# Performance work log

Hardware: AMD Instinct MI355X
Metric: run time of the kernel (lower is better)

## Reference

```python
import jax, jax.numpy as jnp
import numpy as np

B, D = 32768, 1024


def setup_inputs() -> dict:
    key = jax.random.key(0)
    kx, k1, k2, k3 = jax.random.split(key, 4)
    x = jax.random.normal(kx, (B, D), dtype=jnp.float32)
    w1 = jax.random.normal(k1, (D, D), dtype=jnp.float32) * 0.1
    w2 = jax.random.normal(k2, (D, D), dtype=jnp.float32) * 0.1
    w3 = jax.random.normal(k3, (D, D), dtype=jnp.float32) * 0.1
    return {"x": x, "w1": w1, "w2": w2, "w3": w3}


def reference(x, w1, w2, w3):
    # Order 1: plain dense projection
    r1 = jnp.matmul(x, w1)  # [B, D]

    dim = x.shape[1]
    k = int(dim * 0.1)
    # Select top-k facets by mean |x| over the batch
    _, idx = jax.lax.top_k(jnp.abs(x).mean(axis=0), k)  # [k]
    mask = jnp.zeros((dim,), dtype=x.dtype).at[idx].set(1.0)  # [D]

    x_sparse = x * mask  # [B, D], zero outside active facets
    # Order 2: masked matmul, gated elementwise by the sparse input
    r2 = jnp.matmul(x_sparse, w2) * x_sparse
    # Order 3: masked matmul squared, gated elementwise
    r3 = jnp.square(jnp.matmul(x_sparse, w3)) * x_sparse
    return (r1, r2, r3)
```

## Files before the change

kernel.cpp:

```cpp
#include <hip/hip_runtime.h>
#include <hip/hip_bf16.h>
#include <stdint.h>

#define B_ROWS 32768
#define DIM    1024
#define KACT   102
#define KPAD   104

typedef short bf16x8 __attribute__((ext_vector_type(8)));
typedef float f32x4  __attribute__((ext_vector_type(4)));

__device__ __forceinline__ unsigned short f2bf(float f) {
  union { float f; unsigned u; } v; v.f = f;
  unsigned u = v.u;
  unsigned r = u + 0x7fffu + ((u >> 16) & 1u);
  return (unsigned short)(r >> 16);
}

#define GLDS(g, l) __builtin_amdgcn_global_load_lds( \
    (__attribute__((address_space(1))) void*)(g),    \
    (__attribute__((address_space(3))) void*)(l), 16, 0, 0)

__global__ __launch_bounds__(256) void k_conv(
    const float* __restrict__ x, unsigned short* __restrict__ xb,
    float* __restrict__ partial) {
  const int t  = threadIdx.x;
  const int c0 = t * 4;
  const size_t base = (size_t)blockIdx.x * 64 * DIM;
  float s0 = 0.f, s1 = 0.f, s2 = 0.f, s3 = 0.f;
  #pragma unroll 4
  for (int j = 0; j < 64; ++j) {
    size_t off = base + (size_t)j * DIM + c0;
    float4 v = *(const float4*)(x + off);
    s0 += fabsf(v.x); s1 += fabsf(v.y); s2 += fabsf(v.z); s3 += fabsf(v.w);
    ushort4 o;
    o.x = f2bf(v.x); o.y = f2bf(v.y); o.z = f2bf(v.z); o.w = f2bf(v.w);
    *(ushort4*)(xb + off) = o;
  }
  float4 p; p.x = s0; p.y = s1; p.z = s2; p.w = s3;
  *(float4*)(partial + (size_t)blockIdx.x * DIM + c0) = p;
}

__global__ __launch_bounds__(256) void k_w1t(const float* __restrict__ w1,
                                             unsigned short* __restrict__ w1t) {
  __shared__ unsigned short tile[64][65];
  const int t  = threadIdx.x;
  const int bx = blockIdx.x & 15;
  const int by = blockIdx.x >> 4;
  for (int e = t; e < 64 * 64; e += 256) {
    int r = e >> 6, c = e & 63;
    tile[r][c] = f2bf(w1[(size_t)(by * 64 + r) * DIM + bx * 64 + c]);
  }
  __syncthreads();
  for (int e = t; e < 64 * 64; e += 256) {
    int c = e >> 6, r = e & 63;
    w1t[(size_t)(bx * 64 + c) * DIM + by * 64 + r] = tile[r][c];
  }
}

__global__ __launch_bounds__(128) void k_reduce1(const float* __restrict__ partial,
                                                 float* __restrict__ p2) {
  const int c  = (blockIdx.x & 7) * 128 + threadIdx.x;
  const int ks = blockIdx.x >> 3;
  float s = 0.f;
  #pragma unroll 8
  for (int p = ks * 64; p < ks * 64 + 64; ++p) s += partial[(size_t)p * DIM + c];
  p2[ks * DIM + c] = s;
}

__global__ __launch_bounds__(256) void k_rank(const float* __restrict__ p2,
                                              int* __restrict__ flags) {
  __shared__ double sv[DIM];
  const int t = threadIdx.x;
  for (int e = t; e < DIM; e += 256) {
    double s = 0.0;
    #pragma unroll
    for (int ks = 0; ks < 8; ++ks) s += (double)p2[ks * DIM + e];
    sv[e] = s;
  }
  __syncthreads();
  const int d = blockIdx.x * 256 + t;
  const double sd = sv[d];
  int rank = 0;
  for (int j = 0; j < DIM; ++j) {
    double s = sv[j];
    rank += (s > sd || (s == sd && j < d)) ? 1 : 0;
  }
  flags[d] = (rank < KACT) ? 1 : 0;
}

__global__ __launch_bounds__(1024) void k_compact(const int* __restrict__ flags,
                                                  int* __restrict__ act,
                                                  int* __restrict__ cmap) {
  __shared__ int wcnt[16];
  const int d = threadIdx.x;
  const int f = flags[d];
  unsigned long long m = __ballot(f != 0);
  const int lane = d & 63, w = d >> 6;
  if (lane == 0) wcnt[w] = __popcll(m);
  __syncthreads();
  int off = 0;
  for (int i = 0; i < w; ++i) off += wcnt[i];
  int pos = off + __popcll(m & ((1ull << lane) - 1ull));
  cmap[d] = f ? pos : -1;
  if (f) act[pos] = d;
}

__global__ __launch_bounds__(128) void k_wsub(const float* __restrict__ w2,
                                              const float* __restrict__ w3,
                                              const int* __restrict__ act,
                                              float* __restrict__ W2sub,
                                              float* __restrict__ W3sub) {
  const int i = blockIdx.x;
  const int j = threadIdx.x;
  if (j >= KPAD) return;
  float v2 = 0.f, v3 = 0.f;
  if (i < KACT && j < KACT) {
    size_t o = (size_t)act[i] * DIM + act[j];
    v2 = w2[o]; v3 = w3[o];
  }
  W2sub[i * KPAD + j] = v2;
  W3sub[i * KPAD + j] = v3;
}

#define VMW4 asm volatile("s_waitcnt vmcnt(4)" ::: "memory")
#define VMW0 asm volatile("s_waitcnt vmcnt(0)" ::: "memory")
#define NOP_ (void)0

#define STAGE_A(KT) do { \
  GLDS(Abase + (size_t)sr0 * 1024 + (KT) * 32 + sc0 * 8, &Asl[((KT)&3)*8192 + p0*8]); \
  GLDS(Abase + (size_t)sr1 * 1024 + (KT) * 32 + sc1 * 8, &Asl[((KT)&3)*8192 + p1*8]); \
} while (0)
#define STAGE_B(KT) do { \
  GLDS(Bbase + (size_t)sr0 * 1024 + (KT) * 32 + sc0 * 8, &Bsl[((KT)&3)*8192 + p0*8]); \
  GLDS(Bbase + (size_t)sr1 * 1024 + (KT) * 32 + sc1 * 8, &Bsl[((KT)&3)*8192 + p1*8]); \
} while (0)

#define PH0(SLOT, STAGE_STMT) do { \
  _Pragma("unroll") for (int i = 0; i < 4; ++i) \
    areg[i] = *(const bf16x8*)(&Asl[(SLOT)*8192 + aoff0 + i * 512]); \
  _Pragma("unroll") for (int i = 0; i < 4; ++i) \
    breg[i] = *(const bf16x8*)(&Bsl[(SLOT)*8192 + boff0 + i * 512]); \
  STAGE_STMT; \
  __builtin_amdgcn_s_barrier(); \
  __builtin_amdgcn_s_setprio(1); \
  _Pragma("unroll") for (int mi = 0; mi < 4; ++mi) \
  _Pragma("unroll") for (int ni = 0; ni < 4; ++ni) \
    acc[mi][ni] = __builtin_amdgcn_mfma_f32_16x16x32_bf16(areg[mi], breg[ni], acc[mi][ni], 0, 0, 0); \
  __builtin_amdgcn_s_setprio(0); \
  __builtin_amdgcn_s_barrier(); \
} while (0)

#define PH1(SLOT, STAGE_STMT, WAIT_STMT) do { \
  _Pragma("unroll") for (int i = 0; i < 4; ++i) \
    areg[i] = *(const bf16x8*)(&Asl[(SLOT)*8192 + aoff0 + 2048 + i * 512]); \
  STAGE_STMT; \
  WAIT_STMT; \
  __builtin_amdgcn_s_barrier(); \
  __builtin_amdgcn_s_setprio(1); \
  _Pragma("unroll") for (int mi = 0; mi < 4; ++mi) \
  _Pragma("unroll") for (int ni = 0; ni < 4; ++ni) \
    acc[4 + mi][ni] = __builtin_amdgcn_mfma_f32_16x16x32_bf16(areg[mi], breg[ni], acc[4 + mi][ni], 0, 0, 0); \
  __builtin_amdgcn_s_setprio(0); \
  __builtin_amdgcn_s_barrier(); \
} while (0)

__global__ __launch_bounds__(512, 1) void k_gemm_r1(
    const unsigned short* __restrict__ A,
    const unsigned short* __restrict__ Bt,
    float* __restrict__ C) {
  __shared__ unsigned short Asl[4 * 8192];
  __shared__ unsigned short Bsl[4 * 8192];

  const int t    = threadIdx.x;
  const int lane = t & 63;
  const int wave = t >> 6;
  const int wm   = wave >> 2;
  const int wn   = wave & 3;
  const int la   = lane & 15;
  const int kg   = lane >> 4;
  const int kgx  = kg ^ ((la >> 1) & 3);

  const int swz  = (blockIdx.x & 7) * 64 + (blockIdx.x >> 3);
  const int brow = swz >> 2;
  const int bcol = swz & 3;

  const unsigned short* Abase = A  + (size_t)brow * 256 * 1024;
  const unsigned short* Bbase = Bt + (size_t)bcol * 256 * 1024;

  const int p0 = t, p1 = t + 512;
  const int q0 = p0 ^ ((p0 >> 3) & 3);
  const int q1 = p1 ^ ((p1 >> 3) & 3);
  const int sr0 = q0 >> 2, sc0 = q0 & 3;
  const int sr1 = q1 >> 2, sc1 = q1 & 3;

  const int aoff0 = (wm * 128 + la) * 32 + kgx * 8;
  const int boff0 = (wn * 64  + la) * 32 + kgx * 8;

  f32x4 acc[8][4];
  #pragma unroll
  for (int mi = 0; mi < 8; ++mi)
    #pragma unroll
    for (int ni = 0; ni < 4; ++ni)
      acc[mi][ni] = (f32x4){0.f, 0.f, 0.f, 0.f};

  bf16x8 areg[4], breg[4];

  STAGE_A(0); STAGE_B(0); STAGE_A(1); STAGE_B(1);
  VMW4;
  __builtin_amdgcn_s_barrier();

  for (int kt4 = 0; kt4 < 28; kt4 += 4) {
    PH0(0, STAGE_A(kt4 + 2)); PH1(0, STAGE_B(kt4 + 2), VMW4);
    PH0(1, STAGE_A(kt4 + 3)); PH1(1, STAGE_B(kt4 + 3), VMW4);
    PH0(2, STAGE_A(kt4 + 4)); PH1(2, STAGE_B(kt4 + 4), VMW4);
    PH0(3, STAGE_A(kt4 + 5)); PH1(3, STAGE_B(kt4 + 5), VMW4);
  }
  PH0(0, STAGE_A(30)); PH1(0, STAGE_B(30), VMW4);
  PH0(1, STAGE_A(31)); PH1(1, STAGE_B(31), VMW4);
  PH0(2, NOP_);        PH1(2, NOP_, VMW0);
  PH0(3, NOP_);        PH1(3, NOP_, NOP_);

  const int orow0 = brow * 256 + wm * 128 + (lane >> 4) * 4;
  const int ocol0 = bcol * 256 + wn * 64 + la;
  #pragma unroll
  for (int mi = 0; mi < 8; ++mi)
    #pragma unroll
    for (int ni = 0; ni < 4; ++ni)
      #pragma unroll
      for (int r = 0; r < 4; ++r)
        C[(size_t)(orow0 + mi * 16 + r) * DIM + ocol0 + ni * 16] = acc[mi][ni][r];
}

__global__ __launch_bounds__(512) void k_r23(const float* __restrict__ x,
                                             const float* __restrict__ W2sub,
                                             const float* __restrict__ W3sub,
                                             const int* __restrict__ cmap,
                                             float* __restrict__ out2,
                                             float* __restrict__ out3) {
  __shared__ float W2s[KPAD * KPAD];
  __shared__ float W3s[KPAD * KPAD];
  __shared__ float xs[2][16 * KPAD];
  __shared__ float r2s[16 * KPAD];
  __shared__ float r3s[16 * KPAD];
  __shared__ int   cms[DIM];
  const int t    = threadIdx.x;
  const int row0 = blockIdx.x * 128;

  for (int e = t; e < KPAD * KPAD; e += 512) { W2s[e] = W2sub[e]; W3s[e] = W3sub[e]; }
  for (int e = t; e < DIM; e += 512) cms[e] = cmap[e];
  for (int e = t; e < 2 * 16 * KPAD; e += 512) ((float*)xs)[e] = 0.f;
  __syncthreads();

  const int  j   = t & 127;
  const int  rg  = (t >> 7) & 3;
  const bool jok = j < KACT;

  auto LOADR = [&](int ch, f32x4* ld) {
    const size_t base = (size_t)(row0 + ch * 16) * DIM;
    #pragma unroll
    for (int it = 0; it < 8; ++it) {
      int e = t + it * 512;
      int r = e >> 8, c4 = e & 255;
      ld[it] = *(const f32x4*)(x + base + (size_t)r * DIM + c4 * 4);
    }
  };
  auto XSW = [&](int buf, const f32x4* ld) {
    #pragma unroll
    for (int it = 0; it < 8; ++it) {
      int e = t + it * 512;
      int r = e >> 8, c4 = e & 255;
      #pragma unroll
      for (int q = 0; q < 4; ++q) {
        int m = cms[c4 * 4 + q];
        if (m >= 0) xs[buf][r * KPAD + m] = ld[it][q];
      }
    }
  };
  auto COMPUTE = [&](int buf) {
    if (jok) {
      float a2[4], a3[4];
      #pragma unroll
      for (int r = 0; r < 4; ++r) { a2[r] = 0.f; a3[r] = 0.f; }
      for (int i = 0; i < KPAD; i += 4) {
        float w2v[4], w3v[4];
        #pragma unroll
        for (int q = 0; q < 4; ++q) {
          w2v[q] = W2s[(i + q) * KPAD + j];
          w3v[q] = W3s[(i + q) * KPAD + j];
        }
        #pragma unroll
        for (int r = 0; r < 4; ++r) {
          f32x4 xv = *(const f32x4*)(&xs[buf][(rg * 4 + r) * KPAD + i]);
          a2[r] += xv[0] * w2v[0] + xv[1] * w2v[1] + xv[2] * w2v[2] + xv[3] * w2v[3];
          a3[r] += xv[0] * w3v[0] + xv[1] * w3v[1] + xv[2] * w3v[2] + xv[3] * w3v[3];
        }
      }
      #pragma unroll
      for (int r = 0; r < 4; ++r) {
        int rr = rg * 4 + r;
        float g = xs[buf][rr * KPAD + j];
        r2s[rr * KPAD + j] = a2[r] * g;
        r3s[rr * KPAD + j] = a3[r] * a3[r] * g;
      }
    }
  };
  auto WRITEOUT = [&](int ch) {
    const int r0 = row0 + ch * 16;
    const int c0 = (t & 255) * 4;
    const int rh = t >> 8;
    const int4 cm = *(const int4*)(&cms[c0]);
    #pragma unroll
    for (int k = 0; k < 8; ++k) {
      int r = rh + k * 2;
      const float* rr2 = &r2s[r * KPAD];
      const float* rr3 = &r3s[r * KPAD];
      float4 o2, o3;
      o2.x = (cm.x >= 0) ? rr2[cm.x] : 0.f;  o3.x = (cm.x >= 0) ? rr3[cm.x] : 0.f;
      o2.y = (cm.y >= 0) ? rr2[cm.y] : 0.f;  o3.y = (cm.y >= 0) ? rr3[cm.y] : 0.f;
      o2.z = (cm.z >= 0) ? rr2[cm.z] : 0.f;  o3.z = (cm.z >= 0) ? rr3[cm.z] : 0.f;
      o2.w = (cm.w >= 0) ? rr2[cm.w] : 0.f;  o3.w = (cm.w >= 0) ? rr3[cm.w] : 0.f;
      size_t oo = (size_t)(r0 + r) * DIM + c0;
      *(float4*)(out2 + oo) = o2;
      *(float4*)(out3 + oo) = o3;
    }
  };

  f32x4 ldA[8], ldB[8];
  LOADR(0, ldA);
  XSW(0, ldA);
  __syncthreads();
  for (int ch2 = 0; ch2 < 8; ch2 += 2) {
    if (ch2 + 1 < 8) LOADR(ch2 + 1, ldB);
    COMPUTE(0);
    __syncthreads();
    WRITEOUT(ch2);
    if (ch2 + 1 < 8) XSW(1, ldB);
    __syncthreads();
    if (ch2 + 2 < 8) LOADR(ch2 + 2, ldA);
    COMPUTE(1);
    __syncthreads();
    WRITEOUT(ch2 + 1);
    if (ch2 + 2 < 8) XSW(0, ldA);
    __syncthreads();
  }
}

extern "C" void kernel_launch(void* const* d_in, const int* in_sizes, int n_in,
                              void* d_out, int out_size, void* d_ws, size_t ws_size,
                              hipStream_t stream) {
  const float* x  = (const float*)d_in[0];
  const float* w1 = (const float*)d_in[1];
  const float* w2 = (const float*)d_in[2];
  const float* w3 = (const float*)d_in[3];

  float* out1 = (float*)d_out;
  float* out2 = out1 + (size_t)B_ROWS * DIM;
  float* out3 = out2 + (size_t)B_ROWS * DIM;

  char* ws = (char*)d_ws;
  unsigned short* xb     = (unsigned short*)ws;
  unsigned short* w1t    = (unsigned short*)(ws + 67108864);
  float*          partial= (float*)(ws + 69206016);
  float*          p2     = (float*)(ws + 71303168);
  int*            flags  = (int*)(ws + 71335936);
  int*            act    = (int*)(ws + 71340032);
  int*            cmap   = (int*)(ws + 71340544);
  float*          W2sub  = (float*)(ws + 71344640);
  float*          W3sub  = (float*)(ws + 71387904);

  k_conv    <<<dim3(512),  dim3(256),  0, stream>>>(x, xb, partial);
  k_w1t     <<<dim3(256),  dim3(256),  0, stream>>>(w1, w1t);
  k_reduce1 <<<dim3(64),   dim3(128),  0, stream>>>(partial, p2);
  k_rank    <<<dim3(4),    dim3(256),  0, stream>>>(p2, flags);
  k_compact <<<dim3(1),    dim3(1024), 0, stream>>>(flags, act, cmap);
  k_wsub    <<<dim3(KPAD), dim3(128),  0, stream>>>(w2, w3, act, W2sub, W3sub);
  k_gemm_r1 <<<dim3(512),  dim3(512),  0, stream>>>(xb, w1t, out1);
  k_r23     <<<dim3(256),  dim3(512),  0, stream>>>(x, W2sub, W3sub, cmap, out2, out3);
}
```

Baseline: 256.8 us.

## Fuse small prep kernels and feed r2/r3 from bf16 input with packed bf16 weights

Merges the x conversion and w1 transpose into one launch, and folds rank, compaction and submatrix gather into a single-block kernel, cutting launch count. The r2/r3 kernel now reads the bf16 copy of x instead of fp32 and stores W2/W3 submatrices as packed bf16 in shared memory, halving input traffic and LDS footprint so more blocks fit. This trades accuracy: the sparse input and gating values now carry bf16 rounding, which is amplified in the squared term.

New measurement: 267.4 us. +4.1%, slower.

```diff
diff --git a/kernel.cpp b/kernel.cpp
--- a/kernel.cpp
+++ b/kernel.cpp
@@ -6,8 +6,10 @@
 #define DIM    1024
 #define KACT   102
 #define KPAD   104
+#define KP2    53
 
 typedef short bf16x8 __attribute__((ext_vector_type(8)));
+typedef unsigned short u16x8 __attribute__((ext_vector_type(8)));
 typedef float f32x4  __attribute__((ext_vector_type(4)));
 
 __device__ __forceinline__ unsigned short f2bf(float f) {
@@ -16,45 +18,49 @@
   unsigned r = u + 0x7fffu + ((u >> 16) & 1u);
   return (unsigned short)(r >> 16);
 }
+__device__ __forceinline__ float bfasf(unsigned hi16) {
+  union { unsigned u; float f; } v; v.u = hi16;
+  return v.f;
+}
 
 #define GLDS(g, l) __builtin_amdgcn_global_load_lds( \
     (__attribute__((address_space(1))) void*)(g),    \
     (__attribute__((address_space(3))) void*)(l), 16, 0, 0)
 
-__global__ __launch_bounds__(256) void k_conv(
-    const float* __restrict__ x, unsigned short* __restrict__ xb,
+__global__ __launch_bounds__(256) void k_convw(
+    const float* __restrict__ x, const float* __restrict__ w1,
+    unsigned short* __restrict__ xb, unsigned short* __restrict__ w1t,
     float* __restrict__ partial) {
-  const int t  = threadIdx.x;
-  const int c0 = t * 4;
-  const size_t base = (size_t)blockIdx.x * 64 * DIM;
-  float s0 = 0.f, s1 = 0.f, s2 = 0.f, s3 = 0.f;
-  #pragma unroll 4
-  for (int j = 0; j < 64; ++j) {
-    size_t off = base + (size_t)j * DIM + c0;
-    float4 v = *(const float4*)(x + off);
-    s0 += fabsf(v.x); s1 += fabsf(v.y); s2 += fabsf(v.z); s3 += fabsf(v.w);
-    ushort4 o;
-    o.x = f2bf(v.x); o.y = f2bf(v.y); o.z = f2bf(v.z); o.w = f2bf(v.w);
-    *(ushort4*)(xb + off) = o;
-  }
-  float4 p; p.x = s0; p.y = s1; p.z = s2; p.w = s3;
-  *(float4*)(partial + (size_t)blockIdx.x * DIM + c0) = p;
-}
-
-__global__ __launch_bounds__(256) void k_w1t(const float* __restrict__ w1,
-                                             unsigned short* __restrict__ w1t) {
-  __shared__ unsigned short tile[64][65];
-  const int t  = threadIdx.x;
-  const int bx = blockIdx.x & 15;
-  const int by = blockIdx.x >> 4;
-  for (int e = t; e < 64 * 64; e += 256) {
-    int r = e >> 6, c = e & 63;
-    tile[r][c] = f2bf(w1[(size_t)(by * 64 + r) * DIM + bx * 64 + c]);
-  }
-  __syncthreads();
-  for (int e = t; e < 64 * 64; e += 256) {
-    int c = e >> 6, r = e & 63;
-    w1t[(size_t)(bx * 64 + c) * DIM + by * 64 + r] = tile[r][c];
+  const int t = threadIdx.x;
+  if (blockIdx.x < 512) {
+    const int c0 = t * 4;
+    const size_t base = (size_t)blockIdx.x * 64 * DIM;
+    float s0 = 0.f, s1 = 0.f, s2 = 0.f, s3 = 0.f;
+    #pragma unroll 4
+    for (int j = 0; j < 64; ++j) {
+      size_t off = base + (size_t)j * DIM + c0;
+      float4 v = *(const float4*)(x + off);
+      s0 += fabsf(v.x); s1 += fabsf(v.y); s2 += fabsf(v.z); s3 += fabsf(v.w);
+      ushort4 o;
+      o.x = f2bf(v.x); o.y = f2bf(v.y); o.z = f2bf(v.z); o.w = f2bf(v.w);
+      *(ushort4*)(xb + off) = o;
+    }
+    float4 p; p.x = s0; p.y = s1; p.z = s2; p.w = s3;
+    *(float4*)(partial + (size_t)blockIdx.x * DIM + c0) = p;
+  } else {
+    __shared__ unsigned short tile[64][65];
+    const int b  = blockIdx.x - 512;
+    const int bx = b & 15;
+    const int by = b >> 4;
+    for (int e = t; e < 64 * 64; e += 256) {
+      int r = e >> 6, c = e & 63;
+      tile[r][c] = f2bf(w1[(size_t)(by * 64 + r) * DIM + bx * 64 + c]);
+    }
+    __syncthreads();
+    for (int e = t; e < 64 * 64; e += 256) {
+      int c = e >> 6, r = e & 63;
+      w1t[(size_t)(bx * 64 + c) * DIM + by * 64 + r] = tile[r][c];
+    }
   }
 }
 
@@ -68,33 +74,30 @@
   p2[ks * DIM + c] = s;
 }
 
-__global__ __launch_bounds__(256) void k_rank(const float* __restrict__ p2,
-                                              int* __restrict__ flags) {
+__global__ __launch_bounds__(1024) void k_sel(const float* __restrict__ p2,
+                                              const float* __restrict__ w2,
+                                              const float* __restrict__ w3,
+                                              int* __restrict__ cmap,
+                                              float* __restrict__ W2sub,
+                                              float* __restrict__ W3sub) {
   __shared__ double sv[DIM];
-  const int t = threadIdx.x;
-  for (int e = t; e < DIM; e += 256) {
+  __shared__ int wcnt[16];
+  __shared__ int acts[KACT];
+  const int d = threadIdx.x;
+  {
     double s = 0.0;
     #pragma unroll
-    for (int ks = 0; ks < 8; ++ks) s += (double)p2[ks * DIM + e];
-    sv[e] = s;
-  }
-  __syncthreads();
-  const int d = blockIdx.x * 256 + t;
+    for (int ks = 0; ks < 8; ++ks) s += (double)p2[ks * DIM + d];
+    sv[d] = s;
+  }
+  __syncthreads();
   const double sd = sv[d];
   int rank = 0;
   for (int j = 0; j < DIM; ++j) {
     double s = sv[j];
     rank += (s > sd || (s == sd && j < d)) ? 1 : 0;
   }
-  flags[d] = (rank < KACT) ? 1 : 0;
-}
-
-__global__ __launch_bounds__(1024) void k_compact(const int* __restrict__ flags,
-                                                  int* __restrict__ act,
-                                                  int* __restrict__ cmap) {
-  __shared__ int wcnt[16];
-  const int d = threadIdx.x;
-  const int f = flags[d];
+  const int f = (rank < KACT) ? 1 : 0;
   unsigned long long m = __ballot(f != 0);
   const int lane = d & 63, w = d >> 6;
   if (lane == 0) wcnt[w] = __popcll(m);
@@ -103,24 +106,17 @@
   for (int i = 0; i < w; ++i) off += wcnt[i];
   int pos = off + __popcll(m & ((1ull << lane) - 1ull));
   cmap[d] = f ? pos : -1;
-  if (f) act[pos] = d;
-}
-
-__global__ __launch_bounds__(128) void k_wsub(const float* __restrict__ w2,
-                                              const float* __restrict__ w3,
-                                              const int* __restrict__ act,
-                                              float* __restrict__ W2sub,
-                                              float* __restrict__ W3sub) {
-  const int i = blockIdx.x;
-  const int j = threadIdx.x;
-  if (j >= KPAD) return;
-  float v2 = 0.f, v3 = 0.f;
-  if (i < KACT && j < KACT) {
-    size_t o = (size_t)act[i] * DIM + act[j];
-    v2 = w2[o]; v3 = w3[o];
-  }
-  W2sub[i * KPAD + j] = v2;
-  W3sub[i * KPAD + j] = v3;
+  if (f) acts[pos] = d;
+  __syncthreads();
+  for (int e = d; e < KPAD * KPAD; e += 1024) {
+    int i = e / KPAD, j = e - i * KPAD;
+    float v2 = 0.f, v3 = 0.f;
+    if (i < KACT && j < KACT) {
+      size_t o = (size_t)acts[i] * DIM + acts[j];
+      v2 = w2[o]; v3 = w3[o];
+    }
+    W2sub[e] = v2; W3sub[e] = v3;
+  }
 }
 
 #define VMW4 asm volatile("s_waitcnt vmcnt(4)" ::: "memory")
@@ -232,22 +228,31 @@
         C[(size_t)(orow0 + mi * 16 + r) * DIM + ocol0 + ni * 16] = acc[mi][ni][r];
 }
 
-__global__ __launch_bounds__(512) void k_r23(const float* __restrict__ x,
-                                             const float* __restrict__ W2sub,
-                                             const float* __restrict__ W3sub,
-                                             const int* __restrict__ cmap,
-                                             float* __restrict__ out2,
-                                             float* __restrict__ out3) {
-  __shared__ float W2s[KPAD * KPAD];
-  __shared__ float W3s[KPAD * KPAD];
+__global__ __launch_bounds__(512, 4) void k_r23(
+    const unsigned short* __restrict__ xb,
+    const float* __restrict__ W2sub,
+    const float* __restrict__ W3sub,
+    const int* __restrict__ cmap,
+    float* __restrict__ out2,
+    float* __restrict__ out3) {
+  __shared__ unsigned int Wp2[KPAD * KP2];
+  __shared__ unsigned int Wp3[KPAD * KP2];
   __shared__ float xs[2][16 * KPAD];
   __shared__ float r2s[16 * KPAD];
   __shared__ float r3s[16 * KPAD];
   __shared__ int   cms[DIM];
   const int t    = threadIdx.x;
-  const int row0 = blockIdx.x * 128;
-
-  for (int e = t; e < KPAD * KPAD; e += 512) { W2s[e] = W2sub[e]; W3s[e] = W3sub[e]; }
+  const int row0 = blockIdx.x * 64;
+
+  for (int e = t; e < KPAD * 52; e += 512) {
+    int i2 = e / KPAD, j = e - i2 * KPAD;
+    unsigned lo2 = f2bf(W2sub[(2 * i2) * KPAD + j]);
+    unsigned hi2 = f2bf(W2sub[(2 * i2 + 1) * KPAD + j]);
+    Wp2[j * KP2 + i2] = lo2 | (hi2 << 16);
+    unsigned lo3 = f2bf(W3sub[(2 * i2) * KPAD + j]);
+    unsigned hi3 = f2bf(W3sub[(2 * i2 + 1) * KPAD + j]);
+    Wp3[j * KP2 + i2] = lo3 | (hi3 << 16);
+  }
   for (int e = t; e < DIM; e += 512) cms[e] = cmap[e];
   for (int e = t; e < 2 * 16 * KPAD; e += 512) ((float*)xs)[e] = 0.f;
   __syncthreads();
@@ -256,24 +261,24 @@
   const int  rg  = (t >> 7) & 3;
   const bool jok = j < KACT;
 
-  auto LOADR = [&](int ch, f32x4* ld) {
+  auto LOADR = [&](int ch, u16x8* ld) {
     const size_t base = (size_t)(row0 + ch * 16) * DIM;
     #pragma unroll
-    for (int it = 0; it < 8; ++it) {
+    for (int it = 0; it < 4; ++it) {
       int e = t + it * 512;
-      int r = e >> 8, c4 = e & 255;
-      ld[it] = *(const f32x4*)(x + base + (size_t)r * DIM + c4 * 4);
+      int r = e >> 7, c8 = e & 127;
+      ld[it] = *(const u16x8*)(xb + base + (size_t)r * DIM + c8 * 8);
     }
   };
-  auto XSW = [&](int buf, const f32x4* ld) {
-    #pragma unroll
-    for (int it = 0; it < 8; ++it) {
+  auto XSW = [&](int buf, const u16x8* ld) {
+    #pragma unroll
+    for (int it = 0; it < 4; ++it) {
       int e = t + it * 512;
-      int r = e >> 8, c4 = e & 255;
+      int r = e >> 7, c8 = e & 127;
       #pragma unroll
-      for (int q = 0; q < 4; ++q) {
-        int m = cms[c4 * 4 + q];
-        if (m >= 0) xs[buf][r * KPAD + m] = ld[it][q];
+      for (int q = 0; q < 8; ++q) {
+        int m = cms[c8 * 8 + q];
+        if (m >= 0) xs[buf][r * KPAD + m] = bfasf(((unsigned)(unsigned short)ld[it][q]) << 16);
       }
     }
   };
@@ -282,18 +287,20 @@
       float a2[4], a3[4];
       #pragma unroll
       for (int r = 0; r < 4; ++r) { a2[r] = 0.f; a3[r] = 0.f; }
-      for (int i = 0; i < KPAD; i += 4) {
-        float w2v[4], w3v[4];
-        #pragma unroll
-        for (int q = 0; q < 4; ++q) {
-          w2v[q] = W2s[(i + q) * KPAD + j];
-          w3v[q] = W3s[(i + q) * KPAD + j];
-        }
+      const unsigned int* wp2 = &Wp2[j * KP2];
+      const unsigned int* wp3 = &Wp3[j * KP2];
+      for (int g = 0; g < 26; ++g) {
+        unsigned ua = wp2[2 * g], ub = wp2[2 * g + 1];
+        unsigned va = wp3[2 * g], vb = wp3[2 * g + 1];
+        float w2v0 = bfasf(ua << 16), w2v1 = bfasf(ua & 0xFFFF0000u);
+        float w2v2 = bfasf(ub << 16), w2v3 = bfasf(ub & 0xFFFF0000u);
+        float w3v0 = bfasf(va << 16), w3v1 = bfasf(va & 0xFFFF0000u);
+        float w3v2 = bfasf(vb << 16), w3v3 = bfasf(vb & 0xFFFF0000u);
         #pragma unroll
         for (int r = 0; r < 4; ++r) {
-          f32x4 xv = *(const f32x4*)(&xs[buf][(rg * 4 + r) * KPAD + i]);
-          a2[r] += xv[0] * w2v[0] + xv[1] * w2v[1] + xv[2] * w2v[2] + xv[3] * w2v[3];
-          a3[r] += xv[0] * w3v[0] + xv[1] * w3v[1] + xv[2] * w3v[2] + xv[3] * w3v[3];
+          f32x4 xv = *(const f32x4*)(&xs[buf][(rg * 4 + r) * KPAD + g * 4]);
+          a2[r] += xv[0] * w2v0 + xv[1] * w2v1 + xv[2] * w2v2 + xv[3] * w2v3;
+          a3[r] += xv[0] * w3v0 + xv[1] * w3v1 + xv[2] * w3v2 + xv[3] * w3v3;
         }
       }
       #pragma unroll
@@ -326,24 +333,14 @@
     }
   };
 
-  f32x4 ldA[8], ldB[8];
+  u16x8 ldA[4], ldB[4];
   LOADR(0, ldA);
   XSW(0, ldA);
   __syncthreads();
-  for (int ch2 = 0; ch2 < 8; ch2 += 2) {
-    if (ch2 + 1 < 8) LOADR(ch2 + 1, ldB);
-    COMPUTE(0);
-    __syncthreads();
-    WRITEOUT(ch2);
-    if (ch2 + 1 < 8) XSW(1, ldB);
-    __syncthreads();
-    if (ch2 + 2 < 8) LOADR(ch2 + 2, ldA);
-    COMPUTE(1);
-    __syncthreads();
-    WRITEOUT(ch2 + 1);
-    if (ch2 + 2 < 8) XSW(0, ldA);
-    __syncthreads();
-  }
+  LOADR(1, ldB); COMPUTE(0); __syncthreads(); WRITEOUT(0); XSW(1, ldB); __syncthreads();
+  LOADR(2, ldA); COMPUTE(1); __syncthreads(); WRITEOUT(1); XSW(0, ldA); __syncthreads();
+  LOADR(3, ldB); COMPUTE(0); __syncthreads(); WRITEOUT(2); XSW(1, ldB); __syncthreads();
+  COMPUTE(1); __syncthreads(); WRITEOUT(3);
 }
 
 extern "C" void kernel_launch(void* const* d_in, const int* in_sizes, int n_in,
@@ -363,18 +360,13 @@
   unsigned short* w1t    = (unsigned short*)(ws + 67108864);
   float*          partial= (float*)(ws + 69206016);
   float*          p2     = (float*)(ws + 71303168);
-  int*            flags  = (int*)(ws + 71335936);
-  int*            act    = (int*)(ws + 71340032);
-  int*            cmap   = (int*)(ws + 71340544);
-  float*          W2sub  = (float*)(ws + 71344640);
-  float*          W3sub  = (float*)(ws + 71387904);
-
-  k_conv    <<<dim3(512),  dim3(256),  0, stream>>>(x, xb, partial);
-  k_w1t     <<<dim3(256),  dim3(256),  0, stream>>>(w1, w1t);
-  k_reduce1 <<<dim3(64),   dim3(128),  0, stream>>>(partial, p2);
-  k_rank    <<<dim3(4),    dim3(256),  0, stream>>>(p2, flags);
-  k_compact <<<dim3(1),    dim3(1024), 0, stream>>>(flags, act, cmap);
-  k_wsub    <<<dim3(KPAD), dim3(128),  0, stream>>>(w2, w3, act, W2sub, W3sub);
-  k_gemm_r1 <<<dim3(512),  dim3(512),  0, stream>>>(xb, w1t, out1);
-  k_r23     <<<dim3(256),  dim3(512),  0, stream>>>(x, W2sub, W3sub, cmap, out2, out3);
-}
+  int*            cmap   = (int*)(ws + 71335936);
+  float*          W2sub  = (float*)(ws + 71340032);
+  float*          W3sub  = (float*)(ws + 71383296);
+
+  k_convw   <<<dim3(768), dim3(256),  0, stream>>>(x, w1, xb, w1t, partial);
+  k_reduce1 <<<dim3(64),  dim3(128),  0, stream>>>(partial, p2);
+  k_sel     <<<dim3(1),   dim3(1024), 0, stream>>>(p2, w2, w3, cmap, W2sub, W3sub);
+  k_gemm_r1 <<<dim3(512), dim3(512),  0, stream>>>(xb, w1t, out1);
+  k_r23     <<<dim3(512), dim3(512),  0, stream>>>(xb, W2sub, W3sub, cmap, out2, out3);
+}
```
